# Optimization experiments

Hardware: AMD Instinct MI355X
Metric: run time of the kernel (lower is better)

The kernel has to match this reference:

```python
import jax, jax.numpy as jnp
import numpy as np

B, L, A, F = 4096, 12, 768, 4096  # batch, n_layers, d_activations, d_features


def setup_inputs() -> dict:
    key = jax.random.key(0)
    k_x, k_enc, k_dec, k_m, k_s = jax.random.split(key, 5)
    x = jax.random.normal(k_x, (B, L, A), dtype=jnp.float32)
    # Encoder: uniform(-1/sqrt(F), 1/sqrt(F)) per reset_parameters
    enc_thresh = 1.0 / np.sqrt(F)
    W_enc = jax.random.uniform(k_enc, (L, A, F), jnp.float32, -enc_thresh, enc_thresh)
    # Decoder: triangular weights W_i of shape (i+1, F, A), packed along axis 0.
    # Total rows = L*(L+1)//2. uniform(-1/sqrt(A*L), 1/sqrt(A*L)).
    dec_thresh = 1.0 / np.sqrt(A * L)
    n_tri = L * (L + 1) // 2
    W_dec_packed = jax.random.uniform(k_dec, (n_tri, F, A), jnp.float32, -dec_thresh, dec_thresh)
    # JumpReLU threshold per (layer, feature), init 0.03
    theta = jnp.full((L, F), 0.03, dtype=jnp.float32)
    # Dimensionwise input standardizer stats (per layer, per activation dim)
    in_mean = 0.1 * jax.random.normal(k_m, (L, A), dtype=jnp.float32)
    in_std = 1.0 + 0.1 * jax.random.uniform(k_s, (L, A), dtype=jnp.float32)
    return {"x": x, "in_mean": in_mean, "in_std": in_std, "W_enc": W_enc,
            "theta": theta, "W_dec_packed": W_dec_packed}


def reference(x, in_mean, in_std, W_enc, theta, W_dec_packed):
    # Input standardization: (x - mean) / std, broadcast over batch
    sx = (x - in_mean[None]) / in_std[None]                      # [B, L, A]
    # Encoder: per-layer dense projection
    enc = jnp.einsum('bla,laf->blf', sx, W_enc)                  # [B, L, F]
    # JumpReLU: x * (x > theta)
    act = enc * (enc > theta[None]).astype(enc.dtype)            # [B, L, F]
    # Decoder: triangular accumulation. Layer i reads features of layers 0..i
    # with its own weight tensor W_i (slice of the packed triangular buffer).
    n_layers = W_enc.shape[0]
    preds = []
    off = 0
    for i in range(n_layers):
        W_i = W_dec_packed[off:off + i + 1]                      # [i+1, F, A]
        preds.append(jnp.einsum('blf,lfa->ba', act[:, :i + 1], W_i))
        off += i + 1
    logits = jnp.stack(preds, axis=1)                            # [B, L, A]
    # Original forward returns (logits, encoder_out, concat_w_dec); the
    # concat_w_dec list is just a reshape of the decoder params, omitted here.
    return logits, enc
```

## Files before the change

### kernel.cpp

```cpp
#include <hip/hip_runtime.h>
#include <cstdint>
#include <cstddef>

#define B_ 4096
#define L_ 12
#define A_ 768
#define F_ 4096
#define NTRI 78

typedef __bf16 bf16x8 __attribute__((ext_vector_type(8)));
typedef float f32x4 __attribute__((ext_vector_type(4)));
typedef unsigned short u16x4 __attribute__((ext_vector_type(4)));
typedef unsigned short u16x8 __attribute__((ext_vector_type(8)));

__device__ __forceinline__ unsigned short f32_to_bf16(float f) {
  unsigned int u = __float_as_uint(f);
  u += 0x7fffu + ((u >> 16) & 1u);
  return (unsigned short)(u >> 16);
}

__device__ __forceinline__ void gload_lds16(const void* g, void* l) {
  __builtin_amdgcn_global_load_lds(
      (const __attribute__((address_space(1))) void*)g,
      (__attribute__((address_space(3))) void*)l,
      16, 0, 0);
}

__global__ __launch_bounds__(256) void prep_enc_inputs(
    const float* __restrict__ x, const float* __restrict__ mean,
    const float* __restrict__ stdv, unsigned short* __restrict__ sx,
    const float* __restrict__ wenc, unsigned short* __restrict__ wencT) {
  const int bid = blockIdx.x;
  if (bid < 36864) {
    size_t i4 = (size_t)bid * 256 + threadIdx.x;
    size_t e = i4 * 4;
    unsigned int a = (unsigned int)(e % A_);
    unsigned int t = (unsigned int)(e / A_);
    unsigned int b = t / L_;
    unsigned int l = t % L_;
    float4 xv = *(const float4*)(x + e);
    float4 mv = *(const float4*)(mean + (size_t)l * A_ + a);
    float4 sv = *(const float4*)(stdv + (size_t)l * A_ + a);
    u16x4 o;
    o.x = f32_to_bf16((xv.x - mv.x) / sv.x);
    o.y = f32_to_bf16((xv.y - mv.y) / sv.y);
    o.z = f32_to_bf16((xv.z - mv.z) / sv.z);
    o.w = f32_to_bf16((xv.w - mv.w) / sv.w);
    *(u16x4*)(sx + ((size_t)l * B_ + b) * A_ + a) = o;
    return;
  }
  __shared__ float tile[64][65];
  const int tr = bid - 36864;
  const int xq = tr % 12;
  const int rest = tr / 12;
  const int y = rest & 63;
  const int l = rest >> 6;
  const float* inz = wenc + (size_t)l * A_ * F_;
  unsigned short* outz = wencT + (size_t)l * F_ * A_;
  const int r0 = xq * 64;
  const int c0 = y * 64;
  const int t = threadIdx.x;
  {
    const int c = (t & 15) * 4;
    const int rb = t >> 4;
#pragma unroll
    for (int q = 0; q < 4; ++q) {
      const int r = rb + q * 16;
      float4 v = *(const float4*)(inz + (size_t)(r0 + r) * F_ + (c0 + c));
      tile[r][c] = v.x; tile[r][c + 1] = v.y;
      tile[r][c + 2] = v.z; tile[r][c + 3] = v.w;
    }
  }
  __syncthreads();
  {
    const int c = t >> 2;
    const int rb = (t & 3) * 16;
#pragma unroll
    for (int h = 0; h < 2; ++h) {
      u16x8 o;
#pragma unroll
      for (int j = 0; j < 8; ++j) o[j] = f32_to_bf16(tile[rb + h * 8 + j][c]);
      *(u16x8*)(outz + (size_t)(c0 + c) * A_ + (r0 + rb + h * 8)) = o;
    }
  }
}

__global__ __launch_bounds__(256) void transpose_cvt64(
    const float* __restrict__ in, unsigned short* __restrict__ out,
    int R, int C) {
  __shared__ float tile[64][65];
  const float* inz = in + (size_t)blockIdx.z * R * C;
  unsigned short* outz = out + (size_t)blockIdx.z * R * C;
  const int c0 = blockIdx.x * 64, r0 = blockIdx.y * 64;
  const int t = threadIdx.x;
  {
    const int c = (t & 15) * 4;
    const int rb = t >> 4;
#pragma unroll
    for (int q = 0; q < 4; ++q) {
      const int r = rb + q * 16;
      float4 v = *(const float4*)(inz + (size_t)(r0 + r) * C + (c0 + c));
      tile[r][c] = v.x; tile[r][c + 1] = v.y;
      tile[r][c + 2] = v.z; tile[r][c + 3] = v.w;
    }
  }
  __syncthreads();
  {
    const int c = t >> 2;
    const int rb = (t & 3) * 16;
#pragma unroll
    for (int h = 0; h < 2; ++h) {
      u16x8 o;
#pragma unroll
      for (int j = 0; j < 8; ++j) o[j] = f32_to_bf16(tile[rb + h * 8 + j][c]);
      *(u16x8*)(outz + (size_t)(c0 + c) * R + (r0 + rb + h * 8)) = o;
    }
  }
}

template <class KOffA, class KOffB>
__device__ __forceinline__ void gemm_core64(
    int KT, char* AS, char* BS,
    const char* gA0s, const char* gB0s,
    int ldA, int ldB,
    int w, int wr, int wc, int lane,
    KOffA koffA, KOffB koffB, f32x4 (&acc)[8][4]) {
  const int g = lane >> 4;
  const int fr = lane & 15;
  const uint32_t ssr = (uint32_t)((g ^ ((fr >> 1) & 3)) * 16);
  const uint32_t aBase = (uint32_t)(wr * 128 + fr) * 64 + ssr;
  const uint32_t bBase = (uint32_t)(wc * 64 + fr) * 64 + ssr;

  auto stageA = [&](int kt, int h) {
    const uint32_t off = koffA(kt) + (uint32_t)(h * 64);
    char* d = AS + ((kt & 1) << 15) + (h << 14) + (w << 10);
    gload_lds16(gA0s + off, d);
    gload_lds16(gA0s + off + 128u * (uint32_t)ldA, d + 8192);
  };
  auto stageB = [&](int kt, int h) {
    const uint32_t off = koffB(kt) + (uint32_t)(h * 64);
    char* d = BS + ((kt & 1) << 15) + (h << 14) + (w << 10);
    gload_lds16(gB0s + off, d);
    gload_lds16(gB0s + off + 128u * (uint32_t)ldB, d + 8192);
  };

  stageA(0, 0); stageB(0, 0); stageA(0, 1); stageB(0, 1);
  asm volatile("s_waitcnt vmcnt(4)" ::: "memory");
  __builtin_amdgcn_s_barrier();

  bf16x8 bk[4], aA[4], aB[4];
  auto body = [&](int kt) {
    const char* Ab = AS + ((kt & 1) << 15);
    const char* Bb = BS + ((kt & 1) << 15);
    const bool more = (kt + 1 < KT);
#pragma unroll
    for (int ni = 0; ni < 4; ++ni)
      bk[ni] = *(const bf16x8*)(Bb + bBase + ni * 1024);
#pragma unroll
    for (int mi = 0; mi < 4; ++mi)
      aA[mi] = *(const bf16x8*)(Ab + aBase + mi * 1024);
    if (more) stageA(kt + 1, 0);
    __builtin_amdgcn_s_barrier();
    __builtin_amdgcn_s_setprio(1);
#pragma unroll
    for (int mi = 0; mi < 4; ++mi)
#pragma unroll
      for (int ni = 0; ni < 4; ++ni)
        acc[mi][ni] = __builtin_amdgcn_mfma_f32_16x16x32_bf16(
            aA[mi], bk[ni], acc[mi][ni], 0, 0, 0);
    __builtin_amdgcn_s_setprio(0);
    __builtin_amdgcn_s_barrier();
#pragma unroll
    for (int mi = 0; mi < 4; ++mi)
      aB[mi] = *(const bf16x8*)(Ab + aBase + (4 + mi) * 1024);
    if (more) stageB(kt + 1, 0);
    __builtin_amdgcn_s_barrier();
    __builtin_amdgcn_s_setprio(1);
#pragma unroll
    for (int mi = 0; mi < 4; ++mi)
#pragma unroll
      for (int ni = 0; ni < 4; ++ni)
        acc[mi + 4][ni] = __builtin_amdgcn_mfma_f32_16x16x32_bf16(
            aB[mi], bk[ni], acc[mi + 4][ni], 0, 0, 0);
    __builtin_amdgcn_s_setprio(0);
    if (more) { asm volatile("s_waitcnt vmcnt(4)" ::: "memory"); }
    else      { asm volatile("s_waitcnt vmcnt(0)" ::: "memory"); }
    __builtin_amdgcn_s_barrier();
#pragma unroll
    for (int ni = 0; ni < 4; ++ni)
      bk[ni] = *(const bf16x8*)(Bb + 16384 + bBase + ni * 1024);
#pragma unroll
    for (int mi = 0; mi < 4; ++mi)
      aA[mi] = *(const bf16x8*)(Ab + 16384 + aBase + mi * 1024);
    if (more) stageA(kt + 1, 1);
    __builtin_amdgcn_s_barrier();
    __builtin_amdgcn_s_setprio(1);
#pragma unroll
    for (int mi = 0; mi < 4; ++mi)
#pragma unroll
      for (int ni = 0; ni < 4; ++ni)
        acc[mi][ni] = __builtin_amdgcn_mfma_f32_16x16x32_bf16(
            aA[mi], bk[ni], acc[mi][ni], 0, 0, 0);
    __builtin_amdgcn_s_setprio(0);
    __builtin_amdgcn_s_barrier();
#pragma unroll
    for (int mi = 0; mi < 4; ++mi)
      aB[mi] = *(const bf16x8*)(Ab + 16384 + aBase + (4 + mi) * 1024);
    if (more) stageB(kt + 1, 1);
    __builtin_amdgcn_s_barrier();
    __builtin_amdgcn_s_setprio(1);
#pragma unroll
    for (int mi = 0; mi < 4; ++mi)
#pragma unroll
      for (int ni = 0; ni < 4; ++ni)
        acc[mi + 4][ni] = __builtin_amdgcn_mfma_f32_16x16x32_bf16(
            aB[mi], bk[ni], acc[mi + 4][ni], 0, 0, 0);
    __builtin_amdgcn_s_setprio(0);
    if (more) { asm volatile("s_waitcnt vmcnt(4)" ::: "memory"); }
    __builtin_amdgcn_s_barrier();
  };

  for (int kt = 0; kt < KT; kt += 2) {
    body(kt);
    body(kt + 1);
  }
}

__global__ __launch_bounds__(512, 2) void enc_fused(
    const unsigned short* __restrict__ sxT,
    const unsigned short* __restrict__ wT,
    const float* __restrict__ theta,
    float* __restrict__ enc_out,
    unsigned short* __restrict__ act,
    const float* __restrict__ wdec_in,
    unsigned short* __restrict__ wdecT_out)
{
  extern __shared__ __align__(16) char lds[];
  const int bidx = blockIdx.x;
  const int grp = bidx / 17;
  const int rem = bidx - grp * 17;

  if (rem >= 8) {
    const int tr = grp * 9 + (rem - 8);
    const int y = tr & 63;
    const int z = 24 + (tr >> 6);
    float (*tile)[65] = (float(*)[65])lds;
    const float* inz = wdec_in + (size_t)z * F_ * A_;
    unsigned short* outz = wdecT_out + (size_t)z * F_ * A_;
    const int r0 = y * 64;
    const int t = threadIdx.x;
    for (int xq = 0; xq < 12; ++xq) {
      const int c0 = xq * 64;
      {
        const int c = (t & 15) * 4;
        const int rb = t >> 4;
#pragma unroll
        for (int q = 0; q < 2; ++q) {
          const int r = rb + q * 32;
          float4 v = *(const float4*)(inz + (size_t)(r0 + r) * A_ + (c0 + c));
          tile[r][c] = v.x; tile[r][c + 1] = v.y;
          tile[r][c + 2] = v.z; tile[r][c + 3] = v.w;
        }
      }
      __syncthreads();
      {
        const int c = t >> 3;
        const int rb8 = (t & 7) * 8;
        u16x8 o;
#pragma unroll
        for (int j = 0; j < 8; ++j) o[j] = f32_to_bf16(tile[rb8 + j][c]);
        *(u16x8*)(outz + (size_t)(c0 + c) * F_ + (r0 + rb8)) = o;
      }
      __syncthreads();
    }
    return;
  }

  char* AS = lds;
  char* BS = lds + 65536;
  const int e = grp * 8 + rem;
  const int wg = (e & 7) * 384 + (e >> 3);
  const int l = wg >> 8;
  const int blk = wg & 255;
  const int m0 = (blk & 15) * 256;
  const int n0 = (blk >> 4) * 256;
  const int tid = threadIdx.x;
  const int w = tid >> 6, lane = tid & 63;
  const int wr = w >> 2, wc = w & 3;
  const int srowS = w * 16 + (lane >> 2);
  const int chnkS = ((lane & 3) ^ ((lane >> 3) & 3)) * 16;

  const char* gA0s = (const char*)sxT +
      ((size_t)l * B_ + m0 + srowS) * (A_ * 2) + chnkS;
  const char* gB0s = (const char*)wT +
      ((size_t)l * F_ + n0 + srowS) * (A_ * 2) + chnkS;

  f32x4 acc[8][4] = {};
  auto koffA = [](int kt) { return (uint32_t)kt * 128u; };
  auto koffB = [](int kt) { return (uint32_t)kt * 128u; };
  gemm_core64(A_ / 64, AS, BS, gA0s, gB0s, A_ * 2, A_ * 2, w, wr, wc, lane,
              koffA, koffB, acc);

  const int g = lane >> 4, fr = lane & 15;
#pragma unroll
  for (int ni = 0; ni < 4; ++ni) {
    const int gcol = n0 + wc * 64 + ni * 16 + fr;
    const float th = theta[(size_t)l * F_ + gcol];
#pragma unroll
    for (int mi = 0; mi < 8; ++mi) {
      const int growb = m0 + wr * 128 + mi * 16 + g * 4;
#pragma unroll
      for (int jj = 0; jj < 4; ++jj) {
        const float v = acc[mi][ni][jj];
        const size_t grow = (size_t)(growb + jj);
        enc_out[(grow * L_ + l) * F_ + gcol] = v;
        act[((size_t)l * B_ + grow) * F_ + gcol] =
            (v > th) ? f32_to_bf16(v) : (unsigned short)0;
      }
    }
  }
}

__global__ __launch_bounds__(512, 2) void dec_gemm8(
    const unsigned short* __restrict__ act,
    const unsigned short* __restrict__ wdecT,
    float* __restrict__ logits)
{
  extern __shared__ __align__(16) char lds[];
  char* AS = lds;
  char* BS = lds + 65536;
  const int b = blockIdx.x;
  const int xcd = b & 7;
  const int idx = b >> 3;
  const int z = idx / 6;
  const int j = idx - z * 6;
  const int i = 11 - z;
  const int blk = xcd * 6 + j;
  const int m0 = (blk & 15) * 256;
  const int n0 = (blk >> 4) * 256;
  const int triBase = i * (i + 1) / 2;
  const int KT = (i + 1) * 64;
  const int tid = threadIdx.x;
  const int w = tid >> 6, lane = tid & 63;
  const int wr = w >> 2, wc = w & 3;
  const int srowS = w * 16 + (lane >> 2);
  const int chnkS = ((lane & 3) ^ ((lane >> 3) & 3)) * 16;

  const char* gA0s =
      (const char*)act + ((size_t)(m0 + srowS)) * (F_ * 2) + chnkS;
  const char* gB0s = (const char*)wdecT +
      ((size_t)(triBase * A_ + n0 + srowS)) * (F_ * 2) + chnkS;

  f32x4 acc[8][4] = {};
  auto koffA = [](int kt) {
    return (uint32_t)(kt >> 6) * (uint32_t)(B_ * F_ * 2) +
           (uint32_t)(kt & 63) * 128u;
  };
  auto koffB = [](int kt) {
    return (uint32_t)(kt >> 6) * (uint32_t)(A_ * F_ * 2) +
           (uint32_t)(kt & 63) * 128u;
  };
  gemm_core64(KT, AS, BS, gA0s, gB0s, F_ * 2, F_ * 2, w, wr, wc, lane,
              koffA, koffB, acc);

  const int g = lane >> 4, fr = lane & 15;
#pragma unroll
  for (int mi = 0; mi < 8; ++mi) {
    const int growb = m0 + wr * 128 + mi * 16 + g * 4;
#pragma unroll
    for (int ni = 0; ni < 4; ++ni) {
      const int gcol = n0 + wc * 64 + ni * 16 + fr;
#pragma unroll
      for (int jj = 0; jj < 4; ++jj)
        logits[((size_t)(growb + jj) * L_ + i) * A_ + gcol] = acc[mi][ni][jj];
    }
  }
}

extern "C" void kernel_launch(void* const* d_in, const int* in_sizes, int n_in,
                              void* d_out, int out_size, void* d_ws,
                              size_t ws_size, hipStream_t stream) {
  (void)in_sizes; (void)n_in; (void)out_size; (void)ws_size;
  const float* x = (const float*)d_in[0];
  const float* mean = (const float*)d_in[1];
  const float* stdv = (const float*)d_in[2];
  const float* Wenc = (const float*)d_in[3];
  const float* theta = (const float*)d_in[4];
  const float* Wdec = (const float*)d_in[5];

  float* logits = (float*)d_out;
  float* enc = (float*)d_out + (size_t)B_ * L_ * A_;

  char* ws = (char*)d_ws;
  const size_t actBytes = (size_t)L_ * B_ * F_ * 2;
  const size_t sxBytes = (size_t)L_ * B_ * A_ * 2;
  unsigned short* act = (unsigned short*)ws;
  unsigned short* sx = (unsigned short*)(ws + actBytes);
  unsigned short* wencT = (unsigned short*)(ws + actBytes + sxBytes);
  unsigned short* wdecT = (unsigned short*)(ws + actBytes);

  hipFuncSetAttribute((const void*)enc_fused,
                      hipFuncAttributeMaxDynamicSharedMemorySize, 131072);
  hipFuncSetAttribute((const void*)dec_gemm8,
                      hipFuncAttributeMaxDynamicSharedMemorySize, 131072);

  prep_enc_inputs<<<46080, 256, 0, stream>>>(x, mean, stdv, sx, Wenc, wencT);
  enc_fused<<<6528, 512, 131072, stream>>>(sx, wencT, theta, enc, act,
                                           Wdec, wdecT);
  transpose_cvt64<<<dim3(A_ / 64, F_ / 64, 24), 256, 0, stream>>>(
      Wdec, wdecT, F_, A_);
  dec_gemm8<<<576, 512, 131072, stream>>>(act, wdecT, logits);
}
```

Measured before the change: 2.731 ms.

## Split long triangular decoder K-ranges into balanced jobs with partial-sum fixup

```diff
diff --git a/kernel.cpp b/kernel.cpp
--- a/kernel.cpp
+++ b/kernel.cpp
@@ -319,6 +319,108 @@
       }
     }
   }
+}
+
+__constant__ int dec_jobtab[18][4] = {
+  {11, 0, 6, -1}, {11, 6, 12, 0}, {10, 0, 6, -1}, {5, 0, 6, -1},
+  {10, 6, 11, 1}, {9, 0, 5, -1}, {9, 5, 10, 2}, {8, 0, 5, -1},
+  {4, 0, 5, -1},
+  {8, 5, 9, 3}, {7, 0, 4, -1}, {7, 4, 8, 4}, {6, 0, 4, -1},
+  {3, 0, 4, -1},
+  {6, 4, 7, 5}, {2, 0, 3, -1},
+  {1, 0, 2, -1},
+  {0, 0, 1, -1}
+};
+
+__global__ __launch_bounds__(512, 2) void dec_gemm8_split(
+    const unsigned short* __restrict__ act,
+    const unsigned short* __restrict__ wdecT,
+    float* __restrict__ logits,
+    float* __restrict__ partial)
+{
+  extern __shared__ __align__(16) char lds[];
+  char* AS = lds;
+  char* BS = lds + 65536;
+  const int b = blockIdx.x;
+  const int jt = b / 48;
+  const int blk = b - jt * 48;
+  const int i = dec_jobtab[jt][0];
+  const int l0 = dec_jobtab[jt][1];
+  const int l1 = dec_jobtab[jt][2];
+  const int p = dec_jobtab[jt][3];
+  const int m0 = (blk & 15) * 256;
+  const int n0 = (blk >> 4) * 256;
+  const int triBase = i * (i + 1) / 2 + l0;
+  const int KT = (l1 - l0) * 64;
+  const int tid = threadIdx.x;
+  const int w = tid >> 6, lane = tid & 63;
+  const int wr = w >> 2, wc = w & 3;
+  const int srowS = w * 16 + (lane >> 2);
+  const int chnkS = ((lane & 3) ^ ((lane >> 3) & 3)) * 16;
+
+  const char* gA0s = (const char*)act +
+      ((size_t)l0 * B_ + m0 + srowS) * (F_ * 2) + chnkS;
+  const char* gB0s = (const char*)wdecT +
+      ((size_t)triBase * A_ + n0 + srowS) * (F_ * 2) + chnkS;
+
+  f32x4 acc[8][4] = {};
+  auto koffA = [](int kt) {
+    return (uint32_t)(kt >> 6) * (uint32_t)(B_ * F_ * 2) +
+           (uint32_t)(kt & 63) * 128u;
+  };
+  auto koffB = [](int kt) {
+    return (uint32_t)(kt >> 6) * (uint32_t)(A_ * F_ * 2) +
+           (uint32_t)(kt & 63) * 128u;
+  };
+  gemm_core64(KT, AS, BS, gA0s, gB0s, F_ * 2, F_ * 2, w, wr, wc, lane,
+              koffA, koffB, acc);
+
+  const int g = lane >> 4, fr = lane & 15;
+  if (p < 0) {
+#pragma unroll
+    for (int mi = 0; mi < 8; ++mi) {
+      const int growb = m0 + wr * 128 + mi * 16 + g * 4;
+#pragma unroll
+      for (int ni = 0; ni < 4; ++ni) {
+        const int gcol = n0 + wc * 64 + ni * 16 + fr;
+#pragma unroll
+        for (int jj = 0; jj < 4; ++jj)
+          logits[((size_t)(growb + jj) * L_ + i) * A_ + gcol] =
+              acc[mi][ni][jj];
+      }
+    }
+  } else {
+    float* pb = partial + (size_t)p * B_ * A_;
+#pragma unroll
+    for (int mi = 0; mi < 8; ++mi) {
+      const int growb = m0 + wr * 128 + mi * 16 + g * 4;
+#pragma unroll
+      for (int ni = 0; ni < 4; ++ni) {
+        const int gcol = n0 + wc * 64 + ni * 16 + fr;
+#pragma unroll
+        for (int jj = 0; jj < 4; ++jj)
+          pb[(size_t)(growb + jj) * A_ + gcol] = acc[mi][ni][jj];
+      }
+    }
+  }
+}
+
+__global__ __launch_bounds__(256) void dec_fixup(
+    float* __restrict__ logits, const float* __restrict__ partial) {
+  size_t e4 = (size_t)blockIdx.x * 256 + threadIdx.x;
+  const size_t tot = (size_t)6 * B_ * A_ / 4;
+  if (e4 >= tot) return;
+  size_t e = e4 * 4;
+  int p = (int)(e / ((size_t)B_ * A_));
+  size_t r = e - (size_t)p * B_ * A_;
+  int bb = (int)(r / A_);
+  int a = (int)(r - (size_t)bb * A_);
+  const int i = 11 - p;
+  float4 pv = *(const float4*)(partial + e);
+  float* dst = logits + ((size_t)bb * L_ + i) * A_ + a;
+  float4 dv = *(const float4*)dst;
+  dv.x += pv.x; dv.y += pv.y; dv.z += pv.z; dv.w += pv.w;
+  *(float4*)dst = dv;
 }
 
 __global__ __launch_bounds__(512, 2) void dec_gemm8(
@@ -380,7 +482,7 @@
 extern "C" void kernel_launch(void* const* d_in, const int* in_sizes, int n_in,
                               void* d_out, int out_size, void* d_ws,
                               size_t ws_size, hipStream_t stream) {
-  (void)in_sizes; (void)n_in; (void)out_size; (void)ws_size;
+  (void)in_sizes; (void)n_in; (void)out_size;
   const float* x = (const float*)d_in[0];
   const float* mean = (const float*)d_in[1];
   const float* stdv = (const float*)d_in[2];
@@ -394,12 +496,18 @@
   char* ws = (char*)d_ws;
   const size_t actBytes = (size_t)L_ * B_ * F_ * 2;
   const size_t sxBytes = (size_t)L_ * B_ * A_ * 2;
+  const size_t wdecTBytes = (size_t)NTRI * A_ * F_ * 2;
   unsigned short* act = (unsigned short*)ws;
   unsigned short* sx = (unsigned short*)(ws + actBytes);
   unsigned short* wencT = (unsigned short*)(ws + actBytes + sxBytes);
   unsigned short* wdecT = (unsigned short*)(ws + actBytes);
+  float* partial = (float*)(ws + actBytes + wdecTBytes);
+  const size_t partialBytes = (size_t)6 * B_ * A_ * 4;
+  const bool canSplit = ws_size >= actBytes + wdecTBytes + partialBytes;
 
   hipFuncSetAttribute((const void*)enc_fused,
+                      hipFuncAttributeMaxDynamicSharedMemorySize, 131072);
+  hipFuncSetAttribute((const void*)dec_gemm8_split,
                       hipFuncAttributeMaxDynamicSharedMemorySize, 131072);
   hipFuncSetAttribute((const void*)dec_gemm8,
                       hipFuncAttributeMaxDynamicSharedMemorySize, 131072);
@@ -409,5 +517,11 @@
                                            Wdec, wdecT);
   transpose_cvt64<<<dim3(A_ / 64, F_ / 64, 24), 256, 0, stream>>>(
       Wdec, wdecT, F_, A_);
-  dec_gemm8<<<576, 512, 131072, stream>>>(act, wdecT, logits);
-}
+  if (canSplit) {
+    dec_gemm8_split<<<864, 512, 131072, stream>>>(act, wdecT, logits, partial);
+    dec_fixup<<<(6 * B_ * A_ / 4 + 255) / 256, 256, 0, stream>>>(logits,
+                                                                 partial);
+  } else {
+    dec_gemm8<<<576, 512, 131072, stream>>>(act, wdecT, logits);
+  }
+}
```

After: 2.858 ms. 1.05x slower.
